# Kernel tuning notes

Hardware: AMD Instinct MI355X
Metric: run time of the kernel (lower is better)

## Reference

```python
import jax, jax.numpy as jnp
import numpy as np

N_NODES = 50000
N_EDGES = 1600000
NIN = 64
NATT = 64
NHEAD = 4
D_K = NATT // NHEAD  # 16


def setup_inputs() -> dict:
    key = jax.random.key(0)
    ks = jax.random.split(key, 9)
    x = jax.random.normal(ks[0], (N_NODES, NIN), dtype=jnp.float32)
    edge = jax.random.randint(ks[1], (2, N_EDGES), 0, N_NODES, dtype=jnp.int32)
    s = 0.05
    Wq = jax.random.normal(ks[2], (NIN, NATT), dtype=jnp.float32) * s
    bq = jax.random.normal(ks[3], (NATT,), dtype=jnp.float32) * s
    Wk = jax.random.normal(ks[4], (NIN, NATT), dtype=jnp.float32) * s
    bk = jax.random.normal(ks[5], (NATT,), dtype=jnp.float32) * s
    Wv = jax.random.normal(ks[6], (NIN, NATT), dtype=jnp.float32) * s
    bv = jax.random.normal(ks[7], (NATT,), dtype=jnp.float32) * s
    return {"x": x, "edge": edge, "Wq": Wq, "bq": bq, "Wk": Wk, "bk": bk,
            "Wv": Wv, "bv": bv}


def _heads(h):
    # [N, natt] -> view(-1, nhead, d_k).transpose(1, 2) -> [N, d_k, nhead]
    n = h.shape[0]
    return h.reshape(n, NHEAD, D_K).transpose(0, 2, 1)


def reference(x, edge, Wq, bq, Wk, bk, Wv, bv):
    n = x.shape[0]
    q = _heads(x @ Wq + bq)  # [N, d_k, nhead]
    k = _heads(x @ Wk + bk)
    v = _heads(x @ Wv + bv)

    src = q[edge[0]]    # [E, d_k, nhead] gather by source node
    dst_k = k[edge[1]]  # [E, d_k, nhead] gather by destination node

    # scaled dot product over the d_k axis -> [E, nhead]
    prods = jnp.sum(src * dst_k, axis=1) / jnp.sqrt(jnp.float32(D_K))

    # segment softmax grouped by edge[attention_norm_idx] (= edge[0])
    seg = edge[0]
    seg_max = jax.ops.segment_max(prods, seg, num_segments=n)      # [N, nhead]
    ex = jnp.exp(prods - seg_max[seg])                              # [E, nhead]
    denom = jax.ops.segment_sum(ex, seg, num_segments=n)           # [N, nhead]
    attention = ex / (denom[seg] + jnp.float32(1e-16))

    return attention, v, prods
```

## Files before the change

kernel.cpp:

```cpp
#include <hip/hip_runtime.h>
#include <hip/hip_bf16.h>

#define NHEAD 4

typedef __hip_bfloat16 bf16;
typedef __hip_bfloat162 bf162;

__global__ __launch_bounds__(256) void qkv_kernel(
    const float* __restrict__ x,
    const float* __restrict__ Wq, const float* __restrict__ bq,
    const float* __restrict__ Wk, const float* __restrict__ bk,
    const float* __restrict__ Wv, const float* __restrict__ bv,
    bf16* __restrict__ qout, bf16* __restrict__ kout,
    float* __restrict__ vout, int n_nodes) {
  __shared__ float xs[16][64];
  const int t = threadIdx.x;
  const int base = blockIdx.x * 16;
#pragma unroll
  for (int j = 0; j < 4; ++j) {
    const int idx = t + 256 * j;
    const int nn = idx >> 6, cc = idx & 63;
    xs[nn][cc] = (base + nn < n_nodes) ? x[(size_t)(base + nn) * 64 + cc] : 0.f;
  }
  __syncthreads();
  const int c = t & 63;
  const int qg = t >> 6;

  float aq[4], ak[4], av[4];
  const float bqv = bq[c], bkv = bk[c], bvv = bv[c];
#pragma unroll
  for (int j = 0; j < 4; ++j) { aq[j] = bqv; ak[j] = bkv; av[j] = bvv; }

#pragma unroll 4
  for (int r = 0; r < 64; ++r) {
    const float wq = Wq[r * 64 + c];
    const float wk = Wk[r * 64 + c];
    const float wv = Wv[r * 64 + c];
#pragma unroll
    for (int j = 0; j < 4; ++j) {
      const float xv = xs[qg * 4 + j][r];
      aq[j] = fmaf(xv, wq, aq[j]);
      ak[j] = fmaf(xv, wk, ak[j]);
      av[j] = fmaf(xv, wv, av[j]);
    }
  }
#pragma unroll
  for (int j = 0; j < 4; ++j) {
    const int node = base + qg * 4 + j;
    if (node < n_nodes) {
      qout[(size_t)node * 64 + c] = __float2bfloat16(aq[j]);
      kout[(size_t)node * 64 + c] = __float2bfloat16(ak[j]);
      vout[(size_t)node * 64 + (c & 15) * 4 + (c >> 4)] = av[j];
    }
  }
}

__device__ __forceinline__ float dot8(uint4 a, uint4 b) {
  const unsigned* pa = &a.x;
  const unsigned* pb = &b.x;
  float acc = 0.f;
#pragma unroll
  for (int i = 0; i < 4; ++i) {
    const float2 fa = __bfloat1622float2(*(const bf162*)&pa[i]);
    const float2 fb = __bfloat1622float2(*(const bf162*)&pb[i]);
    acc = fmaf(fa.x, fb.x, acc);
    acc = fmaf(fa.y, fb.y, acc);
  }
  return acc;
}

__global__ __launch_bounds__(256) void edge_kernel(
    const int* __restrict__ edge0, const int* __restrict__ edge1,
    const uint4* __restrict__ q, const uint4* __restrict__ k,
    float* __restrict__ prods, float* __restrict__ denom, int n_edges) {
  const long long i = (long long)blockIdx.x * 256 + threadIdx.x;
  const int e = (int)(i >> 2);
  const int h = (int)(i & 3);
  if (e >= n_edges) return;
  const int src = edge0[e];
  const int dst = edge1[e];

  const uint4 a0 = q[(size_t)src * 8 + h * 2];
  const uint4 a1 = q[(size_t)src * 8 + h * 2 + 1];
  const uint4 b0 = k[(size_t)dst * 8 + h * 2];
  const uint4 b1 = k[(size_t)dst * 8 + h * 2 + 1];

  const float p = (dot8(a0, b0) + dot8(a1, b1)) * 0.25f;
  prods[i] = p;
  atomicAdd(&denom[src * 4 + h], __expf(p));
}

__global__ __launch_bounds__(256) void norm_kernel(
    const int* __restrict__ edge0, const float* __restrict__ denom,
    const float* __restrict__ prods, float* __restrict__ attn, long long n4) {
  const long long i = (long long)blockIdx.x * 256 + threadIdx.x;
  if (i >= n4) return;
  const int e = (int)(i >> 2);
  const int h = (int)(i & 3);
  const int seg = edge0[e];
  attn[i] = __expf(prods[i]) / (denom[seg * 4 + h] + 1e-16f);
}

extern "C" void kernel_launch(void* const* d_in, const int* in_sizes, int n_in,
                              void* d_out, int out_size, void* d_ws, size_t ws_size,
                              hipStream_t stream) {
  const float* x  = (const float*)d_in[0];
  const int* edge = (const int*)d_in[1];
  const float* Wq = (const float*)d_in[2];
  const float* bq = (const float*)d_in[3];
  const float* Wk = (const float*)d_in[4];
  const float* bk = (const float*)d_in[5];
  const float* Wv = (const float*)d_in[6];
  const float* bv = (const float*)d_in[7];

  const int n_nodes = in_sizes[0] / 64;
  const int n_edges = in_sizes[1] / 2;
  const int* edge0 = edge;
  const int* edge1 = edge + n_edges;

  float* out_attn  = (float*)d_out;
  float* out_v     = out_attn + (long long)n_edges * NHEAD;
  float* out_prods = out_v + (long long)n_nodes * 64;

  bf16* ws_q = (bf16*)d_ws;
  bf16* ws_k = ws_q + (size_t)n_nodes * 64;
  float* ws_denom = (float*)(ws_k + (size_t)n_nodes * 64);

  hipMemsetAsync(ws_denom, 0, (size_t)n_nodes * NHEAD * sizeof(float), stream);

  {
    const int blocks = (n_nodes + 15) / 16;
    qkv_kernel<<<blocks, 256, 0, stream>>>(x, Wq, bq, Wk, bk, Wv, bv,
                                           ws_q, ws_k, out_v, n_nodes);
  }
  {
    const long long total = (long long)n_edges * NHEAD;
    const int blocks = (int)((total + 255) / 256);
    edge_kernel<<<blocks, 256, 0, stream>>>(edge0, edge1,
                                            (const uint4*)ws_q, (const uint4*)ws_k,
                                            out_prods, ws_denom, n_edges);
    norm_kernel<<<blocks, 256, 0, stream>>>(edge0, ws_denom, out_prods,
                                            out_attn, total);
  }
}
```

Before: 218.7 us.

## Fuse denom zeroing into qkv, dual-edge ILP, vectorize norm per edge

Zeroes the softmax denominator inside the qkv kernel instead of a separate memset. The edge kernel processes two edges per thread to expose more memory-level parallelism. The norm kernel now handles one edge per thread with float4 loads and stores, so each edge index is read once instead of four times. Nontemporal hints are added for streamed data. Together these target launch overhead and redundant or narrow memory traffic.

```diff
diff --git a/kernel.cpp b/kernel.cpp
--- a/kernel.cpp
+++ b/kernel.cpp
@@ -5,6 +5,7 @@
 
 typedef __hip_bfloat16 bf16;
 typedef __hip_bfloat162 bf162;
+typedef float f32x4 __attribute__((ext_vector_type(4)));
 
 __global__ __launch_bounds__(256) void qkv_kernel(
     const float* __restrict__ x,
@@ -12,7 +13,10 @@
     const float* __restrict__ Wk, const float* __restrict__ bk,
     const float* __restrict__ Wv, const float* __restrict__ bv,
     bf16* __restrict__ qout, bf16* __restrict__ kout,
-    float* __restrict__ vout, int n_nodes) {
+    float* __restrict__ vout, float* __restrict__ denom, int n_nodes) {
+  const long long gtid = (long long)blockIdx.x * 256 + threadIdx.x;
+  if (gtid < (long long)n_nodes * NHEAD) denom[gtid] = 0.f;
+
   __shared__ float xs[16][64];
   const int t = threadIdx.x;
   const int base = blockIdx.x * 16;
@@ -20,7 +24,9 @@
   for (int j = 0; j < 4; ++j) {
     const int idx = t + 256 * j;
     const int nn = idx >> 6, cc = idx & 63;
-    xs[nn][cc] = (base + nn < n_nodes) ? x[(size_t)(base + nn) * 64 + cc] : 0.f;
+    xs[nn][cc] = (base + nn < n_nodes)
+                     ? __builtin_nontemporal_load(&x[(size_t)(base + nn) * 64 + cc])
+                     : 0.f;
   }
   __syncthreads();
   const int c = t & 63;
@@ -73,32 +79,53 @@
     const int* __restrict__ edge0, const int* __restrict__ edge1,
     const uint4* __restrict__ q, const uint4* __restrict__ k,
     float* __restrict__ prods, float* __restrict__ denom, int n_edges) {
-  const long long i = (long long)blockIdx.x * 256 + threadIdx.x;
-  const int e = (int)(i >> 2);
-  const int h = (int)(i & 3);
-  if (e >= n_edges) return;
-  const int src = edge0[e];
-  const int dst = edge1[e];
+  const int i = blockIdx.x * 256 + threadIdx.x;
+  const int half = (n_edges + 1) >> 1;
+  const int e0 = i >> 2;
+  const int h = i & 3;
+  if (e0 >= half) return;
+  const int e1 = e0 + half;
+  const bool two = (e1 < n_edges);
+  const int eb = two ? e1 : e0;
 
-  const uint4 a0 = q[(size_t)src * 8 + h * 2];
-  const uint4 a1 = q[(size_t)src * 8 + h * 2 + 1];
-  const uint4 b0 = k[(size_t)dst * 8 + h * 2];
-  const uint4 b1 = k[(size_t)dst * 8 + h * 2 + 1];
+  const int src0 = __builtin_nontemporal_load(&edge0[e0]);
+  const int dst0 = __builtin_nontemporal_load(&edge1[e0]);
+  const int src1 = __builtin_nontemporal_load(&edge0[eb]);
+  const int dst1 = __builtin_nontemporal_load(&edge1[eb]);
 
-  const float p = (dot8(a0, b0) + dot8(a1, b1)) * 0.25f;
-  prods[i] = p;
-  atomicAdd(&denom[src * 4 + h], __expf(p));
+  const size_t qb0 = (size_t)src0 * 8 + h * 2;
+  const size_t kb0 = (size_t)dst0 * 8 + h * 2;
+  const size_t qb1 = (size_t)src1 * 8 + h * 2;
+  const size_t kb1 = (size_t)dst1 * 8 + h * 2;
+  const uint4 a00 = q[qb0], a01 = q[qb0 + 1];
+  const uint4 b00 = k[kb0], b01 = k[kb0 + 1];
+  const uint4 a10 = q[qb1], a11 = q[qb1 + 1];
+  const uint4 b10 = k[kb1], b11 = k[kb1 + 1];
+
+  const float p0 = (dot8(a00, b00) + dot8(a01, b01)) * 0.25f;
+  prods[(size_t)e0 * 4 + h] = p0;
+  atomicAdd(&denom[src0 * 4 + h], __expf(p0));
+  if (two) {
+    const float p1 = (dot8(a10, b10) + dot8(a11, b11)) * 0.25f;
+    prods[(size_t)e1 * 4 + h] = p1;
+    atomicAdd(&denom[src1 * 4 + h], __expf(p1));
+  }
 }
 
 __global__ __launch_bounds__(256) void norm_kernel(
     const int* __restrict__ edge0, const float* __restrict__ denom,
-    const float* __restrict__ prods, float* __restrict__ attn, long long n4) {
-  const long long i = (long long)blockIdx.x * 256 + threadIdx.x;
-  if (i >= n4) return;
-  const int e = (int)(i >> 2);
-  const int h = (int)(i & 3);
-  const int seg = edge0[e];
-  attn[i] = __expf(prods[i]) / (denom[seg * 4 + h] + 1e-16f);
+    const f32x4* __restrict__ prods4, f32x4* __restrict__ attn4, int n_edges) {
+  const int e = blockIdx.x * 256 + threadIdx.x;
+  if (e >= n_edges) return;
+  const int seg = __builtin_nontemporal_load(&edge0[e]);
+  const f32x4 p = prods4[e];
+  const f32x4 den = *(const f32x4*)&denom[(size_t)seg * 4];
+  f32x4 a;
+  a.x = __expf(p.x) / (den.x + 1e-16f);
+  a.y = __expf(p.y) / (den.y + 1e-16f);
+  a.z = __expf(p.z) / (den.z + 1e-16f);
+  a.w = __expf(p.w) / (den.w + 1e-16f);
+  __builtin_nontemporal_store(a, &attn4[e]);
 }
 
 extern "C" void kernel_launch(void* const* d_in, const int* in_sizes, int n_in,
@@ -126,20 +153,23 @@
   bf16* ws_k = ws_q + (size_t)n_nodes * 64;
   float* ws_denom = (float*)(ws_k + (size_t)n_nodes * 64);
 
-  hipMemsetAsync(ws_denom, 0, (size_t)n_nodes * NHEAD * sizeof(float), stream);
-
   {
     const int blocks = (n_nodes + 15) / 16;
     qkv_kernel<<<blocks, 256, 0, stream>>>(x, Wq, bq, Wk, bk, Wv, bv,
-                                           ws_q, ws_k, out_v, n_nodes);
+                                           ws_q, ws_k, out_v, ws_denom, n_nodes);
   }
   {
-    const long long total = (long long)n_edges * NHEAD;
+    const int half = (n_edges + 1) >> 1;
+    const long long total = (long long)half * NHEAD;
     const int blocks = (int)((total + 255) / 256);
     edge_kernel<<<blocks, 256, 0, stream>>>(edge0, edge1,
                                             (const uint4*)ws_q, (const uint4*)ws_k,
                                             out_prods, ws_denom, n_edges);
-    norm_kernel<<<blocks, 256, 0, stream>>>(edge0, ws_denom, out_prods,
-                                            out_attn, total);
+  }
+  {
+    const int blocks = (n_edges + 255) / 256;
+    norm_kernel<<<blocks, 256, 0, stream>>>(edge0, ws_denom,
+                                            (const f32x4*)out_prods,
+                                            (f32x4*)out_attn, n_edges);
   }
 }
```

Result: no change. 217.5 us (-0.6%).
